# Performance work log

Measured on AMD Instinct MI355X. Metric: run time of the kernel, lower is better.

Reference implementation:

```python
import jax, jax.numpy as jnp
import numpy as np

N = 100000      # nodes
D_IN = 512      # in_size
D_OUT = 512     # out_size
E = 200000      # edges per etype
EPS = 1e-5      # LayerNorm eps


def setup_inputs() -> dict:
    key = jax.random.key(0)
    ks = jax.random.split(key, 10)
    scale = 1.0 / np.sqrt(D_IN)
    inp = {
        "x": jax.random.normal(ks[0], (N, D_IN), jnp.float32),
        "W0": jax.random.normal(ks[1], (D_OUT, D_IN), jnp.float32) * scale,
        "W1": jax.random.normal(ks[2], (D_OUT, D_IN), jnp.float32) * scale,
        "W2": jax.random.normal(ks[3], (D_OUT, D_IN), jnp.float32) * scale,
        "gamma": jnp.ones((D_OUT,), jnp.float32),
        "beta": jnp.zeros((D_OUT,), jnp.float32),
        "src0": jax.random.randint(ks[4], (E,), 0, N, jnp.int32),
        "dst0": jax.random.randint(ks[5], (E,), 0, N, jnp.int32),
        "src1": jax.random.randint(ks[6], (E,), 0, N, jnp.int32),
        "dst1": jax.random.randint(ks[7], (E,), 0, N, jnp.int32),
        "src2": jax.random.randint(ks[8], (E,), 0, N, jnp.int32),
        "dst2": jax.random.randint(ks[9], (E,), 0, N, jnp.int32),
    }
    return inp


def _segment_mean(msgs, dst, n):
    # per-dst-node mean; 0 for nodes with no incoming edges (DGL fn.mean semantics)
    s = jax.ops.segment_sum(msgs, dst, num_segments=n)
    c = jax.ops.segment_sum(jnp.ones((msgs.shape[0],), msgs.dtype), dst, num_segments=n)
    return s / jnp.maximum(c, 1.0)[:, None]


def reference(x, W0, W1, W2, gamma, beta, src0, dst0, src1, dst1, src2, dst2):
    # relation-specific linear transforms, averaged over etypes sharing the src ntype
    h = (x @ W0.T + x @ W1.T + x @ W2.T) / 3.0            # [N, D_OUT]
    # per-etype copy_u / mean aggregation
    a0 = _segment_mean(h[src0], dst0, N)
    a1 = _segment_mean(h[src1], dst1, N)
    a2 = _segment_mean(h[src2], dst2, N)
    # cross-etype 'mean' reducer
    h_agg = (a0 + a1 + a2) / 3.0
    # LayerNorm(ReLU(h_agg))
    a = jax.nn.relu(h_agg)
    mu = jnp.mean(a, axis=-1, keepdims=True)
    var = jnp.mean(jnp.square(a - mu), axis=-1, keepdims=True)
    return (a - mu) * jax.lax.rsqrt(var + EPS) * gamma + beta
```

## Files before the change

kernel.cpp:

```cpp
#include <hip/hip_runtime.h>
#include <hip/hip_bf16.h>
#include <cstdint>
#include <cstddef>

#define N_NODES 100000
#define DIM 512
#define NE 200000
#define NSB 196
#define NMT 391

typedef __attribute__((ext_vector_type(4))) float floatx4;
typedef __attribute__((ext_vector_type(8))) short shortx8;

__device__ __forceinline__ unsigned short f2bf(float f) {
    union { float f; uint32_t u; } v; v.f = f;
    uint32_t r = v.u + 0x7fff + ((v.u >> 16) & 1);
    return (unsigned short)(r >> 16);
}

__device__ __forceinline__ float bf2f(unsigned short h) {
    union { uint32_t u; float f; } v; v.u = ((uint32_t)h) << 16;
    return v.f;
}

__device__ __forceinline__ shortx8 cvt8(const float4 a, const float4 b) {
    union { __hip_bfloat162 h2[4]; shortx8 s8; } u;
    u.h2[0] = __float22bfloat162_rn(make_float2(a.x, a.y));
    u.h2[1] = __float22bfloat162_rn(make_float2(a.z, a.w));
    u.h2[2] = __float22bfloat162_rn(make_float2(b.x, b.y));
    u.h2[3] = __float22bfloat162_rn(make_float2(b.z, b.w));
    return u.s8;
}

__device__ __forceinline__ void load_lds16(const void* g, void* l) {
    __builtin_amdgcn_global_load_lds(
        (const __attribute__((address_space(1))) uint32_t*)g,
        (__attribute__((address_space(3))) uint32_t*)l, 16, 0, 0);
}

__global__ __launch_bounds__(256) void count_combine_kernel(
    const int* __restrict__ d0, const int* __restrict__ d1,
    const int* __restrict__ d2, int* __restrict__ cnt,
    const float* __restrict__ W0, const float* __restrict__ W1,
    const float* __restrict__ W2, unsigned short* __restrict__ Wc) {
    int t = blockIdx.x * 256 + threadIdx.x;
    if (t < DIM * DIM)
        Wc[t] = f2bf((W0[t] + W1[t] + W2[t]) * (1.0f / 3.0f));
    if (t < 3 * NE) {
        int e = t / NE;
        int i = t - e * NE;
        const int* dp = (e == 0) ? d0 : (e == 1) ? d1 : d2;
        atomicAdd(&cnt[e * N_NODES + dp[i]], 1);
    }
}

__global__ __launch_bounds__(512) void scan1_kernel(
    const int* __restrict__ cnt, int* __restrict__ bsum) {
    int t = threadIdx.x;
    int n = blockIdx.x * 512 + t;
    int rl = 0;
    if (n < N_NODES) rl = cnt[n] + cnt[N_NODES + n] + cnt[2 * N_NODES + n];
    int v = rl;
    #pragma unroll
    for (int off = 32; off > 0; off >>= 1) v += __shfl_xor(v, off);
    __shared__ int ws_[8];
    if ((t & 63) == 0) ws_[t >> 6] = v;
    __syncthreads();
    if (t == 0) {
        int s = 0;
        #pragma unroll
        for (int i = 0; i < 8; ++i) s += ws_[i];
        bsum[blockIdx.x] = s;
    }
}

__global__ __launch_bounds__(512) void scan3_kernel(
    const int* __restrict__ cnt, const int* __restrict__ bsum,
    int* __restrict__ row_start, int* __restrict__ cursor) {
    __shared__ int shb[512];
    __shared__ int sh[512];
    int t = threadIdx.x;
    shb[t] = (t < NSB) ? bsum[t] : 0;
    __syncthreads();
    #pragma unroll
    for (int off = 1; off < 512; off <<= 1) {
        int add = (t >= off) ? shb[t - off] : 0;
        __syncthreads();
        shb[t] += add;
        __syncthreads();
    }
    int n = blockIdx.x * 512 + t;
    int rl = 0;
    if (n < N_NODES) rl = cnt[n] + cnt[N_NODES + n] + cnt[2 * N_NODES + n];
    sh[t] = rl;
    __syncthreads();
    #pragma unroll
    for (int off = 1; off < 512; off <<= 1) {
        int add = (t >= off) ? sh[t - off] : 0;
        __syncthreads();
        sh[t] += add;
        __syncthreads();
    }
    if (n < N_NODES) {
        int bexcl = shb[blockIdx.x] - bsum[blockIdx.x];
        int excl = sh[t] - rl + bexcl;
        row_start[n] = excl;
        cursor[n] = excl;
    }
}

__global__ __launch_bounds__(256) void bin_kernel(
    const int* __restrict__ s0, const int* __restrict__ d0,
    const int* __restrict__ s1, const int* __restrict__ d1,
    const int* __restrict__ s2, const int* __restrict__ d2,
    int* __restrict__ cursor, int* __restrict__ src_tag) {
    int t = blockIdx.x * 256 + threadIdx.x;
    if (t >= 3 * NE) return;
    int e = t / NE;
    int i = t - e * NE;
    const int* sp; const int* dp;
    if (e == 0)      { sp = s0; dp = d0; }
    else if (e == 1) { sp = s1; dp = d1; }
    else             { sp = s2; dp = d2; }
    int d = dp[i];
    int pos = atomicAdd(&cursor[d], 1);
    src_tag[pos] = sp[i] | (e << 30);
}

__global__ __launch_bounds__(512) void gemm_kernel(
    const float* __restrict__ X, const unsigned short* __restrict__ B,
    unsigned short* __restrict__ H, int M) {
    __shared__ alignas(16) unsigned short Bs[128 * 512];
    __shared__ alignas(16) unsigned short As[256 * 32];
    const int tid = threadIdx.x;
    const int lane = tid & 63;
    const int w = tid >> 6;
    const int wr = w >> 1, wc = w & 1;
    const int q = lane >> 4, r = lane & 15;

    const int lid = ((int)blockIdx.x & 7) * 32 + ((int)blockIdx.x >> 3);
    const int nt = lid & 3, mg = lid >> 2;
    const int n0 = nt * 128;

    #pragma unroll
    for (int i = 0; i < 16; ++i) {
        int ch = i * 512 + tid;
        int row = ch >> 6, c = ch & 63;
        int cs = c ^ (row & 7);
        load_lds16(&B[(size_t)(n0 + row) * DIM + cs * 8], &Bs[ch * 8]);
    }

    for (int mt = mg; mt < NMT; mt += 64) {
        const int m0 = mt * 256;
        const float* ap[2];
        unsigned abyte[2];
        #pragma unroll
        for (int i = 0; i < 2; ++i) {
            int row = i * 128 + (tid >> 2);
            int c = tid & 3;
            int cs = c ^ ((row >> 1) & 3);
            abyte[i] = (unsigned)row * 64 + (unsigned)cs * 16;
            int gm = m0 + row; if (gm >= M) gm = M - 1;
            ap[i] = X + (size_t)gm * DIM + c * 8;
        }
        float4 SL[2][2][2];
        #pragma unroll
        for (int p = 0; p < 2; ++p)
            #pragma unroll
            for (int i = 0; i < 2; ++i) {
                SL[p][i][0] = *(const float4*)(ap[i] + p * 32);
                SL[p][i][1] = *(const float4*)(ap[i] + p * 32 + 4);
            }

        floatx4 acc[4][4] = {};
        #pragma unroll
        for (int s = 0; s < 16; ++s) {
            #pragma unroll
            for (int i = 0; i < 2; ++i)
                *(shortx8*)((char*)As + abyte[i]) =
                    cvt8(SL[s & 1][i][0], SL[s & 1][i][1]);
            if (s + 2 < 16) {
                #pragma unroll
                for (int i = 0; i < 2; ++i) {
                    SL[s & 1][i][0] = *(const float4*)(ap[i] + (s + 2) * 32);
                    SL[s & 1][i][1] = *(const float4*)(ap[i] + (s + 2) * 32 + 4);
                }
            }
            __syncthreads();

            shortx8 af[4], bf[4];
            #pragma unroll
            for (int mi = 0; mi < 4; ++mi) {
                int m = wr * 64 + mi * 16 + r;
                af[mi] = *(const shortx8*)((const char*)As +
                         m * 64 + ((q ^ ((m >> 1) & 3)) << 4));
            }
            #pragma unroll
            for (int nj = 0; nj < 4; ++nj) {
                int n = wc * 64 + nj * 16 + r;
                bf[nj] = *(const shortx8*)((const char*)Bs +
                         n * 1024 + (((4 * s + q) ^ (n & 7)) << 4));
            }
            #pragma unroll
            for (int mi = 0; mi < 4; ++mi)
                #pragma unroll
                for (int nj = 0; nj < 4; ++nj)
                    acc[mi][nj] = __builtin_amdgcn_mfma_f32_16x16x32_bf16(
                        af[mi], bf[nj], acc[mi][nj], 0, 0, 0);
            __syncthreads();
        }

        #pragma unroll
        for (int mi = 0; mi < 4; ++mi) {
            #pragma unroll
            for (int rg = 0; rg < 4; ++rg) {
                int gm = m0 + wr * 64 + mi * 16 + q * 4 + rg;
                if (gm < M) {
                    #pragma unroll
                    for (int nj = 0; nj < 4; ++nj)
                        H[(size_t)gm * DIM + n0 + wc * 64 + nj * 16 + r] =
                            f2bf(acc[mi][nj][rg]);
                }
            }
        }
    }
}

__global__ __launch_bounds__(256) void gather_ln_kernel(
    const unsigned short* __restrict__ h, const int* __restrict__ row_start,
    const int* __restrict__ cnt, const int* __restrict__ src_tag,
    const float* __restrict__ gamma, const float* __restrict__ beta,
    float* __restrict__ out) {
    const int lane = threadIdx.x & 63;
    const int n = blockIdx.x * 4 + (threadIdx.x >> 6);
    if (n >= N_NODES) return;
    const int c0 = cnt[n], c1 = cnt[N_NODES + n], c2 = cnt[2 * N_NODES + n];
    const int len = c0 + c1 + c2;
    const float w0 = 1.0f / (3.0f * (float)max(c0, 1));
    const float w1 = 1.0f / (3.0f * (float)max(c1, 1));
    const float w2 = 1.0f / (3.0f * (float)max(c2, 1));
    const int beg = row_start[n];
    const size_t lx = (size_t)lane * 8;
    float acc[8] = {};
    for (int base = 0; base < len; base += 64) {
        int rem = len - base;
        int m = rem < 64 ? rem : 64;
        int tag = (lane < m) ? src_tag[beg + base + lane] : 0;
        int j = 0;
        for (; j + 4 <= m; j += 4) {
            int u0 = __shfl(tag, j),     u1 = __shfl(tag, j + 1);
            int u2 = __shfl(tag, j + 2), u3 = __shfl(tag, j + 3);
            int e0 = ((unsigned)u0) >> 30, e1 = ((unsigned)u1) >> 30;
            int e2 = ((unsigned)u2) >> 30, e3 = ((unsigned)u3) >> 30;
            float g0 = (e0 == 0) ? w0 : ((e0 == 1) ? w1 : w2);
            float g1 = (e1 == 0) ? w0 : ((e1 == 1) ? w1 : w2);
            float g2 = (e2 == 0) ? w0 : ((e2 == 1) ? w1 : w2);
            float g3 = (e3 == 0) ? w0 : ((e3 == 1) ? w1 : w2);
            shortx8 v0 = *(const shortx8*)(h + (size_t)(u0 & 0x3FFFFFFF) * DIM + lx);
            shortx8 v1 = *(const shortx8*)(h + (size_t)(u1 & 0x3FFFFFFF) * DIM + lx);
            shortx8 v2 = *(const shortx8*)(h + (size_t)(u2 & 0x3FFFFFFF) * DIM + lx);
            shortx8 v3 = *(const shortx8*)(h + (size_t)(u3 & 0x3FFFFFFF) * DIM + lx);
            #pragma unroll
            for (int k = 0; k < 8; ++k) {
                acc[k] += bf2f((unsigned short)v0[k]) * g0;
                acc[k] += bf2f((unsigned short)v1[k]) * g1;
                acc[k] += bf2f((unsigned short)v2[k]) * g2;
                acc[k] += bf2f((unsigned short)v3[k]) * g3;
            }
        }
        for (; j < m; ++j) {
            int u = __shfl(tag, j);
            int e = ((unsigned)u) >> 30;
            float wg = (e == 0) ? w0 : ((e == 1) ? w1 : w2);
            shortx8 v = *(const shortx8*)(h + (size_t)(u & 0x3FFFFFFF) * DIM + lx);
            #pragma unroll
            for (int k = 0; k < 8; ++k)
                acc[k] += bf2f((unsigned short)v[k]) * wg;
        }
    }
    float s1_ = 0.0f, s2_ = 0.0f;
    #pragma unroll
    for (int k = 0; k < 8; ++k) {
        float v = fmaxf(acc[k], 0.0f);
        acc[k] = v; s1_ += v; s2_ += v * v;
    }
    #pragma unroll
    for (int off = 1; off < 64; off <<= 1) {
        s1_ += __shfl_xor(s1_, off);
        s2_ += __shfl_xor(s2_, off);
    }
    float mu = s1_ * (1.0f / DIM);
    float var = s2_ * (1.0f / DIM) - mu * mu;
    float rstd = rsqrtf(var + 1e-5f);
    float4 g0 = *(const float4*)(gamma + lane * 8);
    float4 g1 = *(const float4*)(gamma + lane * 8 + 4);
    float4 b0 = *(const float4*)(beta + lane * 8);
    float4 b1 = *(const float4*)(beta + lane * 8 + 4);
    float4 o0, o1;
    o0.x = (acc[0] - mu) * rstd * g0.x + b0.x;
    o0.y = (acc[1] - mu) * rstd * g0.y + b0.y;
    o0.z = (acc[2] - mu) * rstd * g0.z + b0.z;
    o0.w = (acc[3] - mu) * rstd * g0.w + b0.w;
    o1.x = (acc[4] - mu) * rstd * g1.x + b1.x;
    o1.y = (acc[5] - mu) * rstd * g1.y + b1.y;
    o1.z = (acc[6] - mu) * rstd * g1.z + b1.z;
    o1.w = (acc[7] - mu) * rstd * g1.w + b1.w;
    float4* op = (float4*)(out + (size_t)n * DIM + lane * 8);
    op[0] = o0;
    op[1] = o1;
}

extern "C" void kernel_launch(void* const* d_in, const int* in_sizes, int n_in,
                              void* d_out, int out_size, void* d_ws, size_t ws_size,
                              hipStream_t stream) {
    const float* x     = (const float*)d_in[0];
    const float* W0    = (const float*)d_in[1];
    const float* W1    = (const float*)d_in[2];
    const float* W2    = (const float*)d_in[3];
    const float* gamma = (const float*)d_in[4];
    const float* beta  = (const float*)d_in[5];
    const int* s0  = (const int*)d_in[6];
    const int* dd0 = (const int*)d_in[7];
    const int* s1  = (const int*)d_in[8];
    const int* dd1 = (const int*)d_in[9];
    const int* s2  = (const int*)d_in[10];
    const int* dd2 = (const int*)d_in[11];
    float* out = (float*)d_out;

    char* ws = (char*)d_ws;
    size_t off = 0;
    int* cnt = (int*)(ws + off);             off += 3u * N_NODES * 4u;
    int* row_start = (int*)(ws + off);       off += (size_t)N_NODES * 4u;
    int* cursor = (int*)(ws + off);          off += (size_t)N_NODES * 4u;
    int* bsum = (int*)(ws + off);            off += 2048;
    int* src_tag = (int*)(ws + off);         off += (size_t)3 * NE * 4u;
    unsigned short* Wc = (unsigned short*)(ws + off); off += (size_t)DIM * DIM * 2u;
    off = (off + 255) & ~255ull;
    unsigned short* h = (unsigned short*)(ws + off);

    hipMemsetAsync(cnt, 0, (size_t)3 * N_NODES * sizeof(int), stream);

    count_combine_kernel<<<(3 * NE + 255) / 256, 256, 0, stream>>>(
        dd0, dd1, dd2, cnt, W0, W1, W2, Wc);
    scan1_kernel<<<NSB, 512, 0, stream>>>(cnt, bsum);
    scan3_kernel<<<NSB, 512, 0, stream>>>(cnt, bsum, row_start, cursor);
    bin_kernel<<<(3 * NE + 255) / 256, 256, 0, stream>>>(
        s0, dd0, s1, dd1, s2, dd2, cursor, src_tag);

    gemm_kernel<<<256, 512, 0, stream>>>(x, Wc, h, N_NODES);

    gather_ln_kernel<<<(N_NODES + 3) / 4, 256, 0, stream>>>(
        h, row_start, cnt, src_tag, gamma, beta, out);
}
```

Baseline: 594.9 us.

## Restructure GEMM into non-persistent 128x128 tiles with B fragments read from global

After: 631.2 us. 1.06x slower.

```diff
diff --git a/kernel.cpp b/kernel.cpp
--- a/kernel.cpp
+++ b/kernel.cpp
@@ -7,7 +7,6 @@
 #define DIM 512
 #define NE 200000
 #define NSB 196
-#define NMT 391
 
 typedef __attribute__((ext_vector_type(4))) float floatx4;
 typedef __attribute__((ext_vector_type(8))) short shortx8;
@@ -30,12 +29,6 @@
     u.h2[2] = __float22bfloat162_rn(make_float2(b.x, b.y));
     u.h2[3] = __float22bfloat162_rn(make_float2(b.z, b.w));
     return u.s8;
-}
-
-__device__ __forceinline__ void load_lds16(const void* g, void* l) {
-    __builtin_amdgcn_global_load_lds(
-        (const __attribute__((address_space(1))) uint32_t*)g,
-        (__attribute__((address_space(3))) uint32_t*)l, 16, 0, 0);
 }
 
 __global__ __launch_bounds__(256) void count_combine_kernel(
@@ -127,100 +120,96 @@
     src_tag[pos] = sp[i] | (e << 30);
 }
 
-__global__ __launch_bounds__(512) void gemm_kernel(
+__global__ __launch_bounds__(256) void gemm_kernel(
     const float* __restrict__ X, const unsigned short* __restrict__ B,
     unsigned short* __restrict__ H, int M) {
-    __shared__ alignas(16) unsigned short Bs[128 * 512];
-    __shared__ alignas(16) unsigned short As[256 * 32];
+    __shared__ alignas(16) unsigned short As[2][128 * 64];
     const int tid = threadIdx.x;
     const int lane = tid & 63;
     const int w = tid >> 6;
     const int wr = w >> 1, wc = w & 1;
     const int q = lane >> 4, r = lane & 15;
 
-    const int lid = ((int)blockIdx.x & 7) * 32 + ((int)blockIdx.x >> 3);
-    const int nt = lid & 3, mg = lid >> 2;
-    const int n0 = nt * 128;
-
-    #pragma unroll
-    for (int i = 0; i < 16; ++i) {
-        int ch = i * 512 + tid;
-        int row = ch >> 6, c = ch & 63;
-        int cs = c ^ (row & 7);
-        load_lds16(&B[(size_t)(n0 + row) * DIM + cs * 8], &Bs[ch * 8]);
-    }
-
-    for (int mt = mg; mt < NMT; mt += 64) {
-        const int m0 = mt * 256;
-        const float* ap[2];
-        unsigned abyte[2];
-        #pragma unroll
-        for (int i = 0; i < 2; ++i) {
-            int row = i * 128 + (tid >> 2);
-            int c = tid & 3;
-            int cs = c ^ ((row >> 1) & 3);
-            abyte[i] = (unsigned)row * 64 + (unsigned)cs * 16;
-            int gm = m0 + row; if (gm >= M) gm = M - 1;
-            ap[i] = X + (size_t)gm * DIM + c * 8;
-        }
-        float4 SL[2][2][2];
-        #pragma unroll
-        for (int p = 0; p < 2; ++p)
-            #pragma unroll
-            for (int i = 0; i < 2; ++i) {
-                SL[p][i][0] = *(const float4*)(ap[i] + p * 32);
-                SL[p][i][1] = *(const float4*)(ap[i] + p * 32 + 4);
-            }
-
-        floatx4 acc[4][4] = {};
-        #pragma unroll
-        for (int s = 0; s < 16; ++s) {
-            #pragma unroll
-            for (int i = 0; i < 2; ++i)
-                *(shortx8*)((char*)As + abyte[i]) =
-                    cvt8(SL[s & 1][i][0], SL[s & 1][i][1]);
-            if (s + 2 < 16) {
-                #pragma unroll
-                for (int i = 0; i < 2; ++i) {
-                    SL[s & 1][i][0] = *(const float4*)(ap[i] + (s + 2) * 32);
-                    SL[s & 1][i][1] = *(const float4*)(ap[i] + (s + 2) * 32 + 4);
-                }
-            }
-            __syncthreads();
-
-            shortx8 af[4], bf[4];
-            #pragma unroll
-            for (int mi = 0; mi < 4; ++mi) {
-                int m = wr * 64 + mi * 16 + r;
-                af[mi] = *(const shortx8*)((const char*)As +
-                         m * 64 + ((q ^ ((m >> 1) & 3)) << 4));
-            }
-            #pragma unroll
-            for (int nj = 0; nj < 4; ++nj) {
-                int n = wc * 64 + nj * 16 + r;
-                bf[nj] = *(const shortx8*)((const char*)Bs +
-                         n * 1024 + (((4 * s + q) ^ (n & 7)) << 4));
-            }
+    int lid = ((int)blockIdx.x & 7) * 391 + ((int)blockIdx.x >> 3);
+    int mt = lid >> 2, nt = lid & 3;
+    int m0 = mt * 128, n0 = nt * 128;
+
+    const int arow = tid >> 3;
+    const int ac = tid & 7;
+    const int acs = ac ^ (arow & 7);
+    const unsigned abyte = (unsigned)arow * 128 + (unsigned)acs * 16;
+    const float* aptr[4];
+    #pragma unroll
+    for (int i = 0; i < 4; ++i) {
+        int gm = m0 + i * 32 + arow; if (gm >= M) gm = M - 1;
+        aptr[i] = X + (size_t)gm * DIM + ac * 8;
+    }
+    float4 areg[4][2];
+    auto aload = [&](int k0_) {
+        #pragma unroll
+        for (int i = 0; i < 4; ++i) {
+            areg[i][0] = *(const float4*)(aptr[i] + k0_);
+            areg[i][1] = *(const float4*)(aptr[i] + k0_ + 4);
+        }
+    };
+    auto writeA = [&](int buf) {
+        #pragma unroll
+        for (int i = 0; i < 4; ++i)
+            *(shortx8*)((char*)As[buf] + i * 4096 + abyte) =
+                cvt8(areg[i][0], areg[i][1]);
+    };
+
+    const unsigned short* bptr[4];
+    #pragma unroll
+    for (int nj = 0; nj < 4; ++nj)
+        bptr[nj] = B + (size_t)(n0 + wc * 64 + nj * 16 + r) * DIM;
+
+    floatx4 acc[4][4] = {};
+
+    aload(0);
+    writeA(0);
+    aload(64);
+    __syncthreads();
+
+    #pragma unroll
+    for (int t = 0; t < 8; ++t) {
+        const int cur = t & 1;
+        if (t < 7) writeA(cur ^ 1);
+        if (t < 6) aload((t + 2) * 64);
+        shortx8 bf[2][4];
+        #pragma unroll
+        for (int kk = 0; kk < 2; ++kk)
+            #pragma unroll
+            for (int nj = 0; nj < 4; ++nj)
+                bf[kk][nj] = *(const shortx8*)(bptr[nj] + t * 64 + (kk * 4 + q) * 8);
+        #pragma unroll
+        for (int kk = 0; kk < 2; ++kk) {
+            const int sc = ((kk * 4 + q) ^ (r & 7)) * 16;
+            shortx8 af[4];
+            #pragma unroll
+            for (int mi = 0; mi < 4; ++mi)
+                af[mi] = *(const shortx8*)((const char*)As[cur] +
+                         (wr * 64 + mi * 16 + r) * 128 + sc);
             #pragma unroll
             for (int mi = 0; mi < 4; ++mi)
                 #pragma unroll
                 for (int nj = 0; nj < 4; ++nj)
                     acc[mi][nj] = __builtin_amdgcn_mfma_f32_16x16x32_bf16(
-                        af[mi], bf[nj], acc[mi][nj], 0, 0, 0);
-            __syncthreads();
-        }
-
-        #pragma unroll
-        for (int mi = 0; mi < 4; ++mi) {
-            #pragma unroll
-            for (int rg = 0; rg < 4; ++rg) {
-                int gm = m0 + wr * 64 + mi * 16 + q * 4 + rg;
-                if (gm < M) {
-                    #pragma unroll
-                    for (int nj = 0; nj < 4; ++nj)
-                        H[(size_t)gm * DIM + n0 + wc * 64 + nj * 16 + r] =
-                            f2bf(acc[mi][nj][rg]);
-                }
+                        af[mi], bf[kk][nj], acc[mi][nj], 0, 0, 0);
+        }
+        __syncthreads();
+    }
+
+    #pragma unroll
+    for (int mi = 0; mi < 4; ++mi) {
+        #pragma unroll
+        for (int rg = 0; rg < 4; ++rg) {
+            int gm = m0 + wr * 64 + mi * 16 + q * 4 + rg;
+            if (gm < M) {
+                #pragma unroll
+                for (int nj = 0; nj < 4; ++nj)
+                    H[(size_t)gm * DIM + n0 + wc * 64 + nj * 16 + r] =
+                        f2bf(acc[mi][nj][rg]);
             }
         }
     }
@@ -347,7 +336,7 @@
     bin_kernel<<<(3 * NE + 255) / 256, 256, 0, stream>>>(
         s0, dd0, s1, dd1, s2, dd2, cursor, src_tag);
 
-    gemm_kernel<<<256, 512, 0, stream>>>(x, Wc, h, N_NODES);
+    gemm_kernel<<<3128, 256, 0, stream>>>(x, Wc, h, N_NODES);
 
     gather_ln_kernel<<<(N_NODES + 3) / 4, 256, 0, stream>>>(
         h, row_start, cnt, src_tag, gamma, beta, out);
```
